# Kernel tuning notes

Hardware: AMD Instinct MI355X
Metric: run time of the kernel (lower is better)

The kernel has to match this reference:

```python
import jax, jax.numpy as jnp
import numpy as np

R = 48          # n_comp (== n_comp_xy)
X = Y = Z = 300 # world_size
C = 27          # channels
N = 1_000_000   # query points
XYZ_MIN = 0.0
XYZ_MAX = 1.0


def _sample2d(plane, gh, gw):
    """Bilinear grid_sample, align_corners=True.
    plane: [R, H, W]; gh, gw: [N] normalized coords in [-1, 1] indexing H and W.
    Returns [N, R].
    """
    H, W = plane.shape[1], plane.shape[2]
    ih = (gh + 1.0) * 0.5 * (H - 1)
    iw = (gw + 1.0) * 0.5 * (W - 1)
    i0 = jnp.clip(jnp.floor(ih).astype(jnp.int32), 0, H - 1)
    j0 = jnp.clip(jnp.floor(iw).astype(jnp.int32), 0, W - 1)
    i1 = jnp.minimum(i0 + 1, H - 1)
    j1 = jnp.minimum(j0 + 1, W - 1)
    fh = (ih - i0.astype(ih.dtype))[:, None]  # [N,1]
    fw = (iw - j0.astype(iw.dtype))[:, None]
    p00 = plane[:, i0, j0].T  # [N,R]
    p01 = plane[:, i0, j1].T
    p10 = plane[:, i1, j0].T
    p11 = plane[:, i1, j1].T
    top = p00 * (1 - fw) + p01 * fw
    bot = p10 * (1 - fw) + p11 * fw
    return top * (1 - fh) + bot * fh


def _sample1d(vec, g):
    """Linear interp along length dim (width of the [*,*,L,1] torch vec is 1,
    sampled at 0 -> pure 1D interp).  vec: [R, L]; g: [N] in [-1,1] -> [N,R]."""
    L = vec.shape[1]
    ih = (g + 1.0) * 0.5 * (L - 1)
    i0 = jnp.clip(jnp.floor(ih).astype(jnp.int32), 0, L - 1)
    i1 = jnp.minimum(i0 + 1, L - 1)
    f = (ih - i0.astype(ih.dtype))[:, None]
    return vec[:, i0].T * (1 - f) + vec[:, i1].T * f


def setup_inputs() -> dict:
    key = jax.random.key(0)
    ks = jax.random.split(key, 8)
    return {
        "xyz": jax.random.uniform(ks[0], (N, 3), dtype=jnp.float32),
        "xy_plane": jax.random.normal(ks[1], (R, X, Y), dtype=jnp.float32) * 0.1,
        "xz_plane": jax.random.normal(ks[2], (R, X, Z), dtype=jnp.float32) * 0.1,
        "yz_plane": jax.random.normal(ks[3], (R, Y, Z), dtype=jnp.float32) * 0.1,
        "x_vec": jax.random.normal(ks[4], (R, X), dtype=jnp.float32) * 0.1,
        "y_vec": jax.random.normal(ks[5], (R, Y), dtype=jnp.float32) * 0.1,
        "z_vec": jax.random.normal(ks[6], (R, Z), dtype=jnp.float32) * 0.1,
        "f_vec": jax.random.uniform(ks[7], (3 * R, C), dtype=jnp.float32,
                                     minval=-0.1, maxval=0.1),
    }


def reference(xyz, xy_plane, xz_plane, yz_plane, x_vec, y_vec, z_vec, f_vec):
    # normalize to [-1, 1]
    g = (xyz - XYZ_MIN) / (XYZ_MAX - XYZ_MIN) * 2.0 - 1.0  # [N,3]
    gx, gy, gz = g[:, 0], g[:, 1], g[:, 2]
    xy_feat = _sample2d(xy_plane, gx, gy)  # [N,R]
    xz_feat = _sample2d(xz_plane, gx, gz)
    yz_feat = _sample2d(yz_plane, gy, gz)
    x_feat = _sample1d(x_vec, gx)
    y_feat = _sample1d(y_vec, gy)
    z_feat = _sample1d(z_vec, gz)
    feat = jnp.concatenate([xy_feat * z_feat, xz_feat * y_feat, yz_feat * x_feat],
                           axis=-1)  # [N, 3R]
    return feat @ f_vec  # [N, C]
```

## Files before the change

kernel.cpp:

```cpp
#include <hip/hip_runtime.h>

#define RR 48
#define GG 300
#define HW2 (GG * GG)
#define NPLANE (RR * HW2)
#define NVEC (RR * GG)
#define CC 27
#define NBUCK 32768
#define TP 64
#define TPP 65

#define PBLK ((HW2 + 255) / 256)
#define PB3 (3 * PBLK)
#define VBLK ((3 * NVEC + 255) / 256)
#define TROW 260

struct Axis { int i0, i1; float f; };

__device__ __forceinline__ Axis axis_interp(float x) {
  float g = x * 2.0f - 1.0f;
  float ih = (g + 1.0f) * 0.5f * (float)(GG - 1);
  int i0 = (int)floorf(ih);
  i0 = i0 < 0 ? 0 : (i0 > GG - 1 ? GG - 1 : i0);
  int i1 = i0 + 1 > GG - 1 ? GG - 1 : i0 + 1;
  Axis a; a.i0 = i0; a.i1 = i1; a.f = ih - (float)i0;
  return a;
}

__device__ __forceinline__ unsigned part3(unsigned v) {
  unsigned r = 0;
  r |= (v & 1u);
  r |= (v & 2u) << 2;
  r |= (v & 4u) << 4;
  r |= (v & 8u) << 6;
  r |= (v & 16u) << 8;
  return r;
}

__device__ __forceinline__ int morton_key(float x, float y, float z) {
  int qx = (int)(x * 32.0f); qx = qx < 0 ? 0 : (qx > 31 ? 31 : qx);
  int qy = (int)(y * 32.0f); qy = qy < 0 ? 0 : (qy > 31 ? 31 : qy);
  int qz = (int)(z * 32.0f); qz = qz < 0 ? 0 : (qz > 31 ? 31 : qz);
  return (int)(part3((unsigned)qx) | (part3((unsigned)qy) << 1) | (part3((unsigned)qz) << 2));
}

__global__ void __launch_bounds__(256) preprocess_kernel(
    const float* __restrict__ p0, const float* __restrict__ p1, const float* __restrict__ p2,
    float* __restrict__ t0, float* __restrict__ t1, float* __restrict__ t2,
    const float* __restrict__ v0, const float* __restrict__ v1, const float* __restrict__ v2,
    float* __restrict__ tv0, float* __restrict__ tv1, float* __restrict__ tv2,
    const float* __restrict__ xyz, int n, int* __restrict__ offs) {
  __shared__ float tile[RR * TROW];
  int bb = blockIdx.x;
  int t = threadIdx.x;

  if (bb < PB3) {
    int plane = bb / PBLK;
    int chunk = bb - plane * PBLK;
    const float* in = (plane == 0) ? p0 : (plane == 1) ? p1 : p2;
    float* outp = (plane == 0) ? t0 : (plane == 1) ? t1 : t2;
    int base = chunk * 256;
    if (base + 256 <= HW2) {
      int p4 = t & 63;
      int rg = t >> 6;
#pragma unroll 1
      for (int i = 0; i < 12; ++i) {
        int r = i * 4 + rg;
        float4 v = *(const float4*)(in + (size_t)r * HW2 + base + p4 * 4);
        *(float4*)&tile[r * TROW + p4 * 4] = v;
      }
      __syncthreads();
#pragma unroll 1
      for (int jj = 0; jj < 12; ++jj) {
        int hw = ((jj & 3) << 6) + (t >> 2);
        int c4 = ((jj >> 2) << 2) + (t & 3);
        float4 w;
        w.x = tile[(c4 * 4 + 0) * TROW + hw];
        w.y = tile[(c4 * 4 + 1) * TROW + hw];
        w.z = tile[(c4 * 4 + 2) * TROW + hw];
        w.w = tile[(c4 * 4 + 3) * TROW + hw];
        *(float4*)(outp + (size_t)(base + hw) * RR + c4 * 4) = w;
      }
    } else {
      int pos = base + t;
#pragma unroll 1
      for (int r = 0; r < RR; ++r) {
        float v = (pos < HW2) ? in[(size_t)r * HW2 + pos] : 0.f;
        tile[r * TROW + t] = v;
      }
      __syncthreads();
#pragma unroll 1
      for (int k = t; k < 256 * RR; k += 256) {
        int p = k / RR;
        int r = k - p * RR;
        int hw = base + p;
        if (hw < HW2) outp[(size_t)hw * RR + r] = tile[r * TROW + p];
      }
    }
  } else if (bb < PB3 + VBLK) {
    int e = (bb - PB3) * 256 + t;
    if (e < 3 * NVEC) {
      int v = e / NVEC;
      int rem = e - v * NVEC;
      int i = rem / RR;
      int r = rem - i * RR;
      const float* in = (v == 0) ? v0 : (v == 1) ? v1 : v2;
      float* out = (v == 0) ? tv0 : (v == 1) ? tv1 : tv2;
      out[i * RR + r] = in[r * GG + i];
    }
  } else {
    int i = (bb - PB3 - VBLK) * 256 + t;
    if (i < n) {
      atomicAdd(&offs[morton_key(xyz[i * 3], xyz[i * 3 + 1], xyz[i * 3 + 2])], 1);
    }
  }
}

__global__ void __launch_bounds__(1024) scan_kernel(int* __restrict__ offs) {
  __shared__ int part[1024];
  int t = threadIdx.x;
  int base = t * (NBUCK / 1024);
  int loc[NBUCK / 1024];
  int s = 0;
#pragma unroll
  for (int i = 0; i < NBUCK / 1024; ++i) { loc[i] = offs[base + i]; s += loc[i]; }
  part[t] = s;
  __syncthreads();
  for (int off = 1; off < 1024; off <<= 1) {
    int u = (t >= off) ? part[t - off] : 0;
    __syncthreads();
    part[t] += u;
    __syncthreads();
  }
  int excl = (t == 0) ? 0 : part[t - 1];
#pragma unroll
  for (int i = 0; i < NBUCK / 1024; ++i) {
    int c = loc[i];
    offs[base + i] = excl;
    excl += c;
  }
}

__global__ void __launch_bounds__(256) scatter_kernel(const float* __restrict__ xyz, int n,
                                                      int* __restrict__ offs,
                                                      int* __restrict__ sidx,
                                                      float4* __restrict__ sxyz) {
  int i = blockIdx.x * blockDim.x + threadIdx.x;
  if (i >= n) return;
  float x = xyz[i * 3], y = xyz[i * 3 + 1], z = xyz[i * 3 + 2];
  int key = morton_key(x, y, z);
  int pos = atomicAdd(&offs[key], 1);
  if (sxyz) {
    sxyz[pos] = make_float4(x, y, z, __int_as_float(i));
  } else {
    sidx[pos] = i;
  }
}

__device__ __forceinline__ void gather_seg(const float* __restrict__ P, Axis ai, Axis aj,
                                           const float* __restrict__ V, Axis ak,
                                           int r4, float* __restrict__ dst) {
  float fi = ai.f, fj = aj.f, fk = ak.f;
  float w00 = (1.f - fi) * (1.f - fj);
  float w01 = (1.f - fi) * fj;
  float w10 = fi * (1.f - fj);
  float w11 = fi * fj;
  float omk = 1.f - fk;
  float4 q00 = *(const float4*)(P + (ai.i0 * GG + aj.i0) * RR + r4);
  float4 q01 = *(const float4*)(P + (ai.i0 * GG + aj.i1) * RR + r4);
  float4 q10 = *(const float4*)(P + (ai.i1 * GG + aj.i0) * RR + r4);
  float4 q11 = *(const float4*)(P + (ai.i1 * GG + aj.i1) * RR + r4);
  float4 b0 = *(const float4*)(V + ak.i0 * RR + r4);
  float4 b1 = *(const float4*)(V + ak.i1 * RR + r4);
  float t0 = (w00 * q00.x + w01 * q01.x + w10 * q10.x + w11 * q11.x) * (omk * b0.x + fk * b1.x);
  float t1 = (w00 * q00.y + w01 * q01.y + w10 * q10.y + w11 * q11.y) * (omk * b0.y + fk * b1.y);
  float t2 = (w00 * q00.z + w01 * q01.z + w10 * q10.z + w11 * q11.z) * (omk * b0.z + fk * b1.z);
  float t3 = (w00 * q00.w + w01 * q01.w + w10 * q10.w + w11 * q11.w) * (omk * b0.w + fk * b1.w);
  dst[(r4 + 0) * TPP] = t0;
  dst[(r4 + 1) * TPP] = t1;
  dst[(r4 + 2) * TPP] = t2;
  dst[(r4 + 3) * TPP] = t3;
}

__global__ void __launch_bounds__(256, 4) tensorf_fused(
    const float4* __restrict__ sxyz, const int* __restrict__ sidx,
    const float* __restrict__ xyz,
    const float* __restrict__ Txy, const float* __restrict__ Txz, const float* __restrict__ Tyz,
    const float* __restrict__ Tx, const float* __restrict__ Ty, const float* __restrict__ Tz,
    const float* __restrict__ F, float* __restrict__ out, int n, int chunkLen) {
  __shared__ float featT[144 * TPP];
  __shared__ int oiS[TP];
  int b = blockIdx.x;
  int nb = (b & 7) * chunkLen + (b >> 3);
  int base = nb * TP;
  int tid = threadIdx.x;
  int g = tid >> 4;
  int l = tid & 15;

#pragma unroll 1
  for (int it = 0; it < TP / 16; ++it) {
    int pl = (it << 4) + g;
    int sp = base + pl;
    if (sp < n) {
      float x, y, z;
      int oi;
      if (sxyz) {
        float4 p4 = sxyz[sp];
        x = p4.x; y = p4.y; z = p4.z;
        oi = __float_as_int(p4.w);
      } else {
        oi = sidx[sp];
        x = xyz[oi * 3 + 0];
        y = xyz[oi * 3 + 1];
        z = xyz[oi * 3 + 2];
      }
      if (l == 12) oiS[pl] = oi;
      Axis ax = axis_interp(x), ay = axis_interp(y), az = axis_interp(z);
      if (l < 12) {
        int r4 = l << 2;
        float* dst = &featT[pl];
        gather_seg(Txy, ax, ay, Tz, az, r4, dst + 0 * RR * TPP);
        gather_seg(Txz, ax, az, Ty, ay, r4, dst + 1 * RR * TPP);
        gather_seg(Tyz, ay, az, Tx, ax, r4, dst + 2 * RR * TPP);
      }
    }
  }
  __syncthreads();

  int p = tid & (TP - 1);
  int q = __builtin_amdgcn_readfirstlane(tid >> 6);
  int cbase = (q == 3) ? 20 : q * 7;
  const float* Fh = F + cbase;

  float acc[7];
#pragma unroll
  for (int c = 0; c < 7; ++c) acc[c] = 0.f;

#pragma unroll 4
  for (int k = 0; k < 144; ++k) {
    float fv = featT[k * TPP + p];
#pragma unroll
    for (int c = 0; c < 7; ++c) acc[c] = fmaf(fv, Fh[k * CC + c], acc[c]);
  }

  int sp = base + p;
  if (sp < n) {
    int oi = oiS[p];
    float* o = out + (size_t)oi * CC + cbase;
    if (q != 3) o[0] = acc[0];
#pragma unroll
    for (int c = 1; c < 7; ++c) o[c] = acc[c];
  }
}

__global__ void __launch_bounds__(256) tensorf_naive(
    const float* __restrict__ xyz,
    const float* __restrict__ Pxy, const float* __restrict__ Pxz, const float* __restrict__ Pyz,
    const float* __restrict__ Vx, const float* __restrict__ Vy, const float* __restrict__ Vz,
    const float* __restrict__ F, float* __restrict__ out, int n) {
  int idx = blockIdx.x * blockDim.x + threadIdx.x;
  if (idx >= n) return;
  float x = xyz[idx * 3], y = xyz[idx * 3 + 1], z = xyz[idx * 3 + 2];
  Axis ax = axis_interp(x), ay = axis_interp(y), az = axis_interp(z);
  float acc[CC];
#pragma unroll
  for (int c = 0; c < CC; ++c) acc[c] = 0.f;
  const float* Ps[3] = {Pxy, Pxz, Pyz};
  const float* Vs[3] = {Vz, Vy, Vx};
  Axis A[3][2] = {{ax, ay}, {ax, az}, {ay, az}};
  Axis K[3] = {az, ay, ax};
#pragma unroll 1
  for (int s = 0; s < 3; ++s) {
    Axis ai = A[s][0], aj = A[s][1], ak = K[s];
    float fi = ai.f, fj = aj.f, fk = ak.f;
    float w00 = (1.f - fi) * (1.f - fj), w01 = (1.f - fi) * fj;
    float w10 = fi * (1.f - fj), w11 = fi * fj, omk = 1.f - fk;
#pragma unroll 1
    for (int r = 0; r < RR; ++r) {
      const float* pr = Ps[s] + r * HW2;
      float ft = (w00 * pr[ai.i0 * GG + aj.i0] + w01 * pr[ai.i0 * GG + aj.i1] +
                  w10 * pr[ai.i1 * GG + aj.i0] + w11 * pr[ai.i1 * GG + aj.i1]) *
                 (omk * Vs[s][r * GG + ak.i0] + fk * Vs[s][r * GG + ak.i1]);
      const float* Fr = F + (s * RR + r) * CC;
#pragma unroll
      for (int c = 0; c < CC; ++c) acc[c] = fmaf(ft, Fr[c], acc[c]);
    }
  }
  float* o = out + (size_t)idx * CC;
#pragma unroll
  for (int c = 0; c < CC; ++c) o[c] = acc[c];
}

extern "C" void kernel_launch(void* const* d_in, const int* in_sizes, int n_in,
                              void* d_out, int out_size, void* d_ws, size_t ws_size,
                              hipStream_t stream) {
  const float* xyz = (const float*)d_in[0];
  const float* pxy = (const float*)d_in[1];
  const float* pxz = (const float*)d_in[2];
  const float* pyz = (const float*)d_in[3];
  const float* vx = (const float*)d_in[4];
  const float* vy = (const float*)d_in[5];
  const float* vz = (const float*)d_in[6];
  const float* F = (const float*)d_in[7];
  float* out = (float*)d_out;
  int n = in_sizes[0] / 3;
  int nblk = (n + 255) / 256;

  size_t fixed = (size_t)(3 * NPLANE + 3 * NVEC) * sizeof(float) +
                 (size_t)NBUCK * sizeof(int);
  size_t need1 = fixed + (size_t)n * sizeof(int);
  size_t need2 = fixed + (size_t)n * sizeof(float4);

  if (ws_size >= need1) {
    float* w = (float*)d_ws;
    float* Txy = w;
    float* Txz = Txy + NPLANE;
    float* Tyz = Txz + NPLANE;
    float* Tx = Tyz + NPLANE;
    float* Ty = Tx + NVEC;
    float* Tz = Ty + NVEC;
    int* offs = (int*)(Tz + NVEC);

    int* sidx = nullptr;
    float4* sxyz = nullptr;
    if (ws_size >= need2) sxyz = (float4*)(offs + NBUCK);
    else sidx = (int*)(offs + NBUCK);

    hipMemsetAsync(offs, 0, (size_t)NBUCK * sizeof(int), stream);
    preprocess_kernel<<<PB3 + VBLK + nblk, 256, 0, stream>>>(
        pxy, pxz, pyz, Txy, Txz, Tyz, vx, vy, vz, Tx, Ty, Tz, xyz, n, offs);
    scan_kernel<<<1, 1024, 0, stream>>>(offs);
    scatter_kernel<<<nblk, 256, 0, stream>>>(xyz, n, offs, sidx, sxyz);

    int ntile = (n + TP - 1) / TP;
    int chunkLen = (ntile + 7) / 8;
    tensorf_fused<<<chunkLen * 8, 256, 0, stream>>>(sxyz, sidx, xyz, Txy, Txz, Tyz,
                                                    Tx, Ty, Tz, F, out, n, chunkLen);
  } else {
    tensorf_naive<<<nblk, 256, 0, stream>>>(xyz, pxy, pxz, pyz, vx, vy, vz, F, out, n);
  }
}
```

Measured before the change: 538.7 us.

## Fuse plane transpose with scatter and split transpose tiles into row passes

The histogram now runs alone ahead of the scan, and the plane and vector transposes are moved into the same launch as the point scatter so they overlap with it rather than with the histogram. The plane transpose tile shrinks from all 48 ranks to 16-rank passes, which means more blocks with smaller shared memory per block and higher occupancy. The edge case is handled by bounds checks in the fast path instead of a separate slow path. The cost is an extra kernel launch and more blocks that each do less work.

```diff
diff --git a/kernel.cpp b/kernel.cpp
--- a/kernel.cpp
+++ b/kernel.cpp
@@ -10,10 +10,13 @@
 #define TP 64
 #define TPP 65
 
-#define PBLK ((HW2 + 255) / 256)
-#define PB3 (3 * PBLK)
+#define TROWS 16
+#define TCOLS 256
+#define PCHUNK ((HW2 + TCOLS - 1) / TCOLS)
+#define NPASS (RR / TROWS)
+#define TPB3 (3 * NPASS * PCHUNK)
 #define VBLK ((3 * NVEC + 255) / 256)
-#define TROW 260
+#define TROW2 260
 
 struct Axis { int i0, i1; float f; };
 
@@ -44,61 +47,98 @@
   return (int)(part3((unsigned)qx) | (part3((unsigned)qy) << 1) | (part3((unsigned)qz) << 2));
 }
 
-__global__ void __launch_bounds__(256) preprocess_kernel(
+__global__ void __launch_bounds__(256) hist_kernel(const float* __restrict__ xyz, int n,
+                                                   int* __restrict__ offs) {
+  int i = blockIdx.x * blockDim.x + threadIdx.x;
+  if (i >= n) return;
+  atomicAdd(&offs[morton_key(xyz[i * 3], xyz[i * 3 + 1], xyz[i * 3 + 2])], 1);
+}
+
+__global__ void __launch_bounds__(1024) scan_kernel(int* __restrict__ offs) {
+  __shared__ int part[1024];
+  int t = threadIdx.x;
+  int base = t * (NBUCK / 1024);
+  int loc[NBUCK / 1024];
+  int s = 0;
+#pragma unroll
+  for (int i = 0; i < NBUCK / 1024; ++i) { loc[i] = offs[base + i]; s += loc[i]; }
+  part[t] = s;
+  __syncthreads();
+  for (int off = 1; off < 1024; off <<= 1) {
+    int u = (t >= off) ? part[t - off] : 0;
+    __syncthreads();
+    part[t] += u;
+    __syncthreads();
+  }
+  int excl = (t == 0) ? 0 : part[t - 1];
+#pragma unroll
+  for (int i = 0; i < NBUCK / 1024; ++i) {
+    int c = loc[i];
+    offs[base + i] = excl;
+    excl += c;
+  }
+}
+
+__global__ void __launch_bounds__(256) trans_scatter_kernel(
+    const float* __restrict__ xyz, int n, int* __restrict__ offs,
+    int* __restrict__ sidx, float4* __restrict__ sxyz, int scb,
     const float* __restrict__ p0, const float* __restrict__ p1, const float* __restrict__ p2,
     float* __restrict__ t0, float* __restrict__ t1, float* __restrict__ t2,
     const float* __restrict__ v0, const float* __restrict__ v1, const float* __restrict__ v2,
-    float* __restrict__ tv0, float* __restrict__ tv1, float* __restrict__ tv2,
-    const float* __restrict__ xyz, int n, int* __restrict__ offs) {
-  __shared__ float tile[RR * TROW];
+    float* __restrict__ tv0, float* __restrict__ tv1, float* __restrict__ tv2) {
+  __shared__ float tile[TROWS * TROW2];
   int bb = blockIdx.x;
   int t = threadIdx.x;
 
-  if (bb < PB3) {
-    int plane = bb / PBLK;
-    int chunk = bb - plane * PBLK;
+  if (bb < scb) {
+    int i = bb * 256 + t;
+    if (i < n) {
+      float x = xyz[i * 3], y = xyz[i * 3 + 1], z = xyz[i * 3 + 2];
+      int key = morton_key(x, y, z);
+      int pos = atomicAdd(&offs[key], 1);
+      if (sxyz) sxyz[pos] = make_float4(x, y, z, __int_as_float(i));
+      else      sidx[pos] = i;
+    }
+  } else if (bb < scb + TPB3) {
+    int rem = bb - scb;
+    int plane = rem / (NPASS * PCHUNK);
+    rem -= plane * (NPASS * PCHUNK);
+    int pass = rem / PCHUNK;
+    int chunk = rem - pass * PCHUNK;
     const float* in = (plane == 0) ? p0 : (plane == 1) ? p1 : p2;
     float* outp = (plane == 0) ? t0 : (plane == 1) ? t1 : t2;
-    int base = chunk * 256;
-    if (base + 256 <= HW2) {
-      int p4 = t & 63;
-      int rg = t >> 6;
-#pragma unroll 1
-      for (int i = 0; i < 12; ++i) {
-        int r = i * 4 + rg;
-        float4 v = *(const float4*)(in + (size_t)r * HW2 + base + p4 * 4);
-        *(float4*)&tile[r * TROW + p4 * 4] = v;
+    int base = chunk * TCOLS;
+    int rbase = pass * TROWS;
+
+    int p4 = t & 63;
+    int rg = t >> 6;
+#pragma unroll
+    for (int i = 0; i < TROWS / 4; ++i) {
+      int r = i * 4 + rg;
+      int pos = base + p4 * 4;
+      if (pos < HW2) {
+        float4 v = *(const float4*)(in + (size_t)(rbase + r) * HW2 + pos);
+        *(float4*)&tile[r * TROW2 + p4 * 4] = v;
       }
-      __syncthreads();
-#pragma unroll 1
-      for (int jj = 0; jj < 12; ++jj) {
-        int hw = ((jj & 3) << 6) + (t >> 2);
-        int c4 = ((jj >> 2) << 2) + (t & 3);
+    }
+    __syncthreads();
+
+    int c4 = t & 3;
+    int hwl = t >> 2;
+#pragma unroll
+    for (int jj = 0; jj < 4; ++jj) {
+      int hw = jj * 64 + hwl;
+      if (base + hw < HW2) {
         float4 w;
-        w.x = tile[(c4 * 4 + 0) * TROW + hw];
-        w.y = tile[(c4 * 4 + 1) * TROW + hw];
-        w.z = tile[(c4 * 4 + 2) * TROW + hw];
-        w.w = tile[(c4 * 4 + 3) * TROW + hw];
-        *(float4*)(outp + (size_t)(base + hw) * RR + c4 * 4) = w;
+        w.x = tile[(c4 * 4 + 0) * TROW2 + hw];
+        w.y = tile[(c4 * 4 + 1) * TROW2 + hw];
+        w.z = tile[(c4 * 4 + 2) * TROW2 + hw];
+        w.w = tile[(c4 * 4 + 3) * TROW2 + hw];
+        *(float4*)(outp + (size_t)(base + hw) * RR + rbase + c4 * 4) = w;
       }
-    } else {
-      int pos = base + t;
-#pragma unroll 1
-      for (int r = 0; r < RR; ++r) {
-        float v = (pos < HW2) ? in[(size_t)r * HW2 + pos] : 0.f;
-        tile[r * TROW + t] = v;
-      }
-      __syncthreads();
-#pragma unroll 1
-      for (int k = t; k < 256 * RR; k += 256) {
-        int p = k / RR;
-        int r = k - p * RR;
-        int hw = base + p;
-        if (hw < HW2) outp[(size_t)hw * RR + r] = tile[r * TROW + p];
-      }
-    }
-  } else if (bb < PB3 + VBLK) {
-    int e = (bb - PB3) * 256 + t;
+    }
+  } else {
+    int e = (bb - scb - TPB3) * 256 + t;
     if (e < 3 * NVEC) {
       int v = e / NVEC;
       int rem = e - v * NVEC;
@@ -108,52 +148,6 @@
       float* out = (v == 0) ? tv0 : (v == 1) ? tv1 : tv2;
       out[i * RR + r] = in[r * GG + i];
     }
-  } else {
-    int i = (bb - PB3 - VBLK) * 256 + t;
-    if (i < n) {
-      atomicAdd(&offs[morton_key(xyz[i * 3], xyz[i * 3 + 1], xyz[i * 3 + 2])], 1);
-    }
-  }
-}
-
-__global__ void __launch_bounds__(1024) scan_kernel(int* __restrict__ offs) {
-  __shared__ int part[1024];
-  int t = threadIdx.x;
-  int base = t * (NBUCK / 1024);
-  int loc[NBUCK / 1024];
-  int s = 0;
-#pragma unroll
-  for (int i = 0; i < NBUCK / 1024; ++i) { loc[i] = offs[base + i]; s += loc[i]; }
-  part[t] = s;
-  __syncthreads();
-  for (int off = 1; off < 1024; off <<= 1) {
-    int u = (t >= off) ? part[t - off] : 0;
-    __syncthreads();
-    part[t] += u;
-    __syncthreads();
-  }
-  int excl = (t == 0) ? 0 : part[t - 1];
-#pragma unroll
-  for (int i = 0; i < NBUCK / 1024; ++i) {
-    int c = loc[i];
-    offs[base + i] = excl;
-    excl += c;
-  }
-}
-
-__global__ void __launch_bounds__(256) scatter_kernel(const float* __restrict__ xyz, int n,
-                                                      int* __restrict__ offs,
-                                                      int* __restrict__ sidx,
-                                                      float4* __restrict__ sxyz) {
-  int i = blockIdx.x * blockDim.x + threadIdx.x;
-  if (i >= n) return;
-  float x = xyz[i * 3], y = xyz[i * 3 + 1], z = xyz[i * 3 + 2];
-  int key = morton_key(x, y, z);
-  int pos = atomicAdd(&offs[key], 1);
-  if (sxyz) {
-    sxyz[pos] = make_float4(x, y, z, __int_as_float(i));
-  } else {
-    sidx[pos] = i;
   }
 }
 
@@ -327,10 +321,11 @@
     else sidx = (int*)(offs + NBUCK);
 
     hipMemsetAsync(offs, 0, (size_t)NBUCK * sizeof(int), stream);
-    preprocess_kernel<<<PB3 + VBLK + nblk, 256, 0, stream>>>(
-        pxy, pxz, pyz, Txy, Txz, Tyz, vx, vy, vz, Tx, Ty, Tz, xyz, n, offs);
+    hist_kernel<<<nblk, 256, 0, stream>>>(xyz, n, offs);
     scan_kernel<<<1, 1024, 0, stream>>>(offs);
-    scatter_kernel<<<nblk, 256, 0, stream>>>(xyz, n, offs, sidx, sxyz);
+    trans_scatter_kernel<<<nblk + TPB3 + VBLK, 256, 0, stream>>>(
+        xyz, n, offs, sidx, sxyz, nblk,
+        pxy, pxz, pyz, Txy, Txz, Tyz, vx, vy, vz, Tx, Ty, Tz);
 
     int ntile = (n + TP - 1) / TP;
     int chunkLen = (ntile + 7) / 8;
```

After: 544.2 us. No clear change (+1.0%).
